# Optimization experiments

Hardware: AMD Instinct MI355X
Metric: run time of the kernel (lower is better)

The kernel has to match this reference:

```python
import jax, jax.numpy as jnp
import numpy as np


def setup_inputs() -> dict:
    key = jax.random.key(0)
    ks = jax.random.split(key, 4)
    C = 64
    return {
        "x": jax.random.normal(ks[0], (8, 64, 32, 32, 96), jnp.float32),
        "w_sr": jax.random.normal(ks[1], (64,), jnp.float32) * 0.1,
        "b_sr": jnp.zeros((64,), jnp.float32),
        "Wq": jax.random.normal(ks[2], (64, 64), jnp.float32) / np.sqrt(C),
        "bq": jnp.zeros((64,), jnp.float32),
        "Wkv": jax.random.normal(ks[3], (128, 64), jnp.float32) / np.sqrt(C),
        "bkv": jnp.zeros((128,), jnp.float32),
        "gamma": jnp.ones((4,), jnp.float32),
        "beta": jnp.zeros((4,), jnp.float32),
    }


def reference(x, w_sr, b_sr, Wq, bq, Wkv, bkv, gamma, beta):
    B, C, H, W, D = x.shape
    NH = gamma.shape[0]
    hd = C // NH
    scale = hd ** -0.5

    # 1x1x1 conv projections == channel matmuls
    q = jnp.einsum('oc,bchwd->bohwd', Wq, x) + bq[None, :, None, None, None]
    # sr_conv with sr_ratio=1 is a depthwise 1x1x1 conv: per-channel scale+shift
    kvin = x * w_sr[None, :, None, None, None] + b_sr[None, :, None, None, None]
    kv = jnp.einsum('oc,bchwd->bohwd', Wkv, kvin) + bkv[None, :, None, None, None]
    k, v = kv[:, :C], kv[:, C:]

    q = q.reshape(B, NH, hd, H, W, D)
    k = k.reshape(B, NH, hd, H, W, D)
    v = v.reshape(B, NH, hd, H, W, D)

    # Manhattan decay: spatial_dist[i,j] = |i-j| + |j-i| = 2|i-j| (H==W);
    # spectral_dist is identically zero in the original (d_idx.T is a no-op on 1D).
    idx = jnp.arange(H, dtype=x.dtype)
    dist = 2.0 * jnp.abs(idx[:, None] - idx[None, :])              # (H, H)
    dec = dist[None, :, :, None] * gamma[:, None, None, None] + beta[:, None, None, None]  # (NH,H,H,1)
    decay = jnp.exp(-jax.nn.softplus(dec))                          # broadcasts over D

    # matmul contracts over W; head_dim c is batch-like (faithful to original permutes)
    attn = jnp.einsum('bnchwd,bncgwd->bnchgd', q, k) * scale        # (B,NH,hd,H,H,D)
    attn = attn + decay[None, :, None]                               # (1,NH,1,H,H,1)
    attn = jax.nn.softmax(attn, axis=-1)                             # softmax over spectral D
    out = jnp.einsum('bnchgd,bncgjd->bnchjd', attn, v)               # (B,NH,hd,H,W,D)
    return out.reshape(B, C, H, W, D)
```

## Files before the change

kernel.cpp:

```cpp
#include <hip/hip_runtime.h>
#include <stdint.h>
#include <stddef.h>

typedef __attribute__((ext_vector_type(8))) short short8;
typedef __attribute__((ext_vector_type(4))) float f32x4;

#define PER_BO 98304

__device__ __forceinline__ unsigned int cvtpk(float lo, float hi) {
    unsigned int r;
    asm("v_cvt_pk_bf16_f32 %0, %1, %2" : "=v"(r) : "v"(lo), "v"(hi));
    return r;
}

__global__ __launch_bounds__(512, 2) void proj_mfma(
    const float* __restrict__ x, const float* __restrict__ w_sr, const float* __restrict__ b_sr,
    const float* __restrict__ Wq, const float* __restrict__ bq,
    const float* __restrict__ Wkv, const float* __restrict__ bkv,
    unsigned short* __restrict__ qb, unsigned short* __restrict__ kb, unsigned short* __restrict__ vb)
{
    __shared__ unsigned short Wh[12288];
    __shared__ float bl[192];
    __shared__ unsigned short Cb[2 * 6208];

    int t = threadIdx.x;
    int bidx = blockIdx.x;
    int b = bidx & 7;
    int dg = (bidx >> 3) & 7;
    int hrow = bidx >> 6;

    int lane = t & 63;
    int wvi = t >> 6;
    int lr = lane & 15, hk = lane >> 4;

    const float* xb = x + (size_t)b * 6291456 + hrow * 3072 + dg * 12;
    float af[3][16];
#pragma unroll
    for (int pi = 0; pi < 3; ++pi) {
        int m = (wvi * 3 + pi) * 16 + lr;
        int w = m / 12, dd = m - w * 12;
        const float* xp = xb + (size_t)(hk * 8) * 98304 + w * 96 + dd;
#pragma unroll
        for (int j = 0; j < 8; ++j) {
            af[pi][j]     = xp[(size_t)j * 98304];
            af[pi][8 + j] = xp[(size_t)(32 + j) * 98304];
        }
    }

#pragma unroll
    for (int i = 0; i < 6; ++i) {
        int qi = t + i * 512;
        int o = qi >> 4;
        int cq = qi & 15;
        int c = cq * 4;
        float4 wv4;
        if (o < 64) wv4 = *reinterpret_cast<const float4*>(Wq + o * 64 + c);
        else {
            wv4 = *reinterpret_cast<const float4*>(Wkv + (o - 64) * 64 + c);
            float4 sr = *reinterpret_cast<const float4*>(w_sr + c);
            wv4.x *= sr.x; wv4.y *= sr.y; wv4.z *= sr.z; wv4.w *= sr.w;
        }
        uint2 pk; pk.x = cvtpk(wv4.x, wv4.y); pk.y = cvtpk(wv4.z, wv4.w);
        int sw = (cq >> 1) ^ (o & 7);
        *reinterpret_cast<uint2*>(&Wh[o * 64 + sw * 8 + (cq & 1) * 4]) = pk;
    }
    if (t < 192) {
        float s;
        if (t < 64) s = bq[t];
        else {
            s = bkv[t - 64];
            for (int c = 0; c < 64; ++c) s += Wkv[(t - 64) * 64 + c] * b_sr[c];
        }
        bl[t] = s;
    }
    __syncthreads();

    short8 ahf[3][2], alf[3][2];
#pragma unroll
    for (int pi = 0; pi < 3; ++pi) {
#pragma unroll
        for (int half = 0; half < 2; ++half) {
            union { unsigned int u[4]; short8 v; } H, L;
#pragma unroll
            for (int q = 0; q < 4; ++q) {
                float f0 = af[pi][half * 8 + 2 * q];
                float f1 = af[pi][half * 8 + 2 * q + 1];
                unsigned int hp = cvtpk(f0, f1);
                float h0 = __uint_as_float(hp << 16);
                float h1 = __uint_as_float(hp & 0xffff0000u);
                H.u[q] = hp;
                L.u[q] = cvtpk(f0 - h0, f1 - h1);
            }
            ahf[pi][half] = H.v; alf[pi][half] = L.v;
        }
    }

    int wo[3];
#pragma unroll
    for (int pi = 0; pi < 3; ++pi)
        wo[pi] = lr * 388 + (wvi * 3 + pi) * 16 + hk * 4;

    int so_po[3], so_lo[3];
#pragma unroll
    for (int i = 0; i < 3; ++i) {
        int flat = i * 512 + t;
        int o_l = flat / 96;
        int rem = flat - o_l * 96;
        int dd = rem >> 3;
        int w4 = rem & 7;
        so_po[i] = o_l * PER_BO + dd * 1024 + w4 * 4;
        so_lo[i] = o_l * 388 + w4 * 48 + dd;
    }

    float biasv[12];
#pragma unroll
    for (int ot = 0; ot < 12; ++ot) biasv[ot] = bl[ot * 16 + lr];

    f32x4 zero4 = {0.f, 0.f, 0.f, 0.f};
    int s7 = lr & 7;

#pragma unroll
    for (int ot = 0; ot < 12; ++ot) {
        unsigned short* cb = Cb + (ot & 1) * 6208;
        {
            int o = ot * 16 + lr;
            const unsigned short* wr = &Wh[o * 64];
            short8 b0 = *reinterpret_cast<const short8*>(wr + ((hk ^ s7) * 8));
            short8 b1 = *reinterpret_cast<const short8*>(wr + (((hk + 4) ^ s7) * 8));
            float bo = biasv[ot];
#pragma unroll
            for (int pi = 0; pi < 3; ++pi) {
                f32x4 acc = __builtin_amdgcn_mfma_f32_16x16x32_bf16(ahf[pi][0], b0, zero4, 0, 0, 0);
                acc = __builtin_amdgcn_mfma_f32_16x16x32_bf16(ahf[pi][1], b1, acc, 0, 0, 0);
                acc = __builtin_amdgcn_mfma_f32_16x16x32_bf16(alf[pi][0], b0, acc, 0, 0, 0);
                acc = __builtin_amdgcn_mfma_f32_16x16x32_bf16(alf[pi][1], b1, acc, 0, 0, 0);
                uint2 st;
                st.x = cvtpk(acc[0] + bo, acc[1] + bo);
                st.y = cvtpk(acc[2] + bo, acc[3] + bo);
                *reinterpret_cast<uint2*>(&cb[wo[pi]]) = st;
            }
        }
        __syncthreads();
        {
            int sel = ot >> 2;
            unsigned short* base =
                (sel == 0 ? qb : (sel == 1 ? kb : vb))
                + (size_t)(b * 64 + (ot & 3) * 16) * PER_BO + dg * 12288 + hrow * 32;
#pragma unroll
            for (int i = 0; i < 3; ++i) {
                const unsigned short* c = &cb[so_lo[i]];
                uint2 v;
                v.x = (unsigned int)c[0]  | ((unsigned int)c[12] << 16);
                v.y = (unsigned int)c[24] | ((unsigned int)c[36] << 16);
                *reinterpret_cast<uint2*>(base + so_po[i]) = v;
            }
        }
    }
}

__global__ __launch_bounds__(512, 4) void attn_kernel(
    const unsigned short* __restrict__ qb, const unsigned short* __restrict__ kb,
    const unsigned short* __restrict__ vb,
    const float* __restrict__ gamma, const float* __restrict__ beta,
    float* __restrict__ out)
{
    __shared__ char smem[61440];
    unsigned short* Vw = (unsigned short*)smem;
    unsigned short* Pb = (unsigned short*)(smem + 18432);
    float* Osf  = (float*)(smem + 27648);
    float* lred = (float*)(smem + 27648);
    float* rlb  = (float*)(smem + 27648 + 16896);

    int t = threadIdx.x;
    int l = t & 63;
    int dsub = t >> 6;
    int lr = l & 15, hk = l >> 4;

    int id = blockIdx.x;
    int xcd = id & 7;
    int k7 = id >> 3;
    int p = xcd + 8 * (k7 >> 1);
    int half = k7 & 1;
    int oc = p & 63;
    int b = p >> 6;
    int n = oc >> 4;

    const unsigned short* qp = qb + (size_t)(b * 64 + oc) * PER_BO;
    const unsigned short* kp = kb + (size_t)(b * 64 + oc) * PER_BO;
    const unsigned short* vp = vb + (size_t)(b * 64 + oc) * PER_BO;

    float gm = gamma[n], bt = beta[n];
    float decv[8];
#pragma unroll
    for (int gb = 0; gb < 2; ++gb)
#pragma unroll
        for (int r = 0; r < 4; ++r) {
            int hh = half * 16 + hk * 4 + r;
            int gg = gb * 16 + lr;
            float dc = 2.0f * fabsf((float)(hh - gg)) * gm + bt;
            float sp = fmaxf(dc, 0.0f) + log1pf(__expf(-fabsf(dc)));
            decv[gb * 4 + r] = __expf(-sp);
        }

    const float scale = 0.25f;
    f32x4 zero4 = {0.f, 0.f, 0.f, 0.f};

    unsigned int ep[48];
    float lacc[8] = {0.f, 0.f, 0.f, 0.f, 0.f, 0.f, 0.f, 0.f};

    int qoff  = half * 512 + lr * 32 + hk * 8;
    int koff0 = lr * 32 + hk * 8;
    int koff1 = koff0 + 512;

    uint4 qv[2], k0v[2], k1v[2];
    {
        int b0p = dsub * 1024;
        qv[0]  = *reinterpret_cast<const uint4*>(qp + b0p + qoff);
        k0v[0] = *reinterpret_cast<const uint4*>(kp + b0p + koff0);
        k1v[0] = *reinterpret_cast<const uint4*>(kp + b0p + koff1);
        int b1p = (8 + dsub) * 1024;
        qv[1]  = *reinterpret_cast<const uint4*>(qp + b1p + qoff);
        k0v[1] = *reinterpret_cast<const uint4*>(kp + b1p + koff0);
        k1v[1] = *reinterpret_cast<const uint4*>(kp + b1p + koff1);
    }

#pragma unroll
    for (int ch = 0; ch < 12; ++ch) {
        int s = ch & 1;
        union { uint4 u; short8 v; } A, B0, B1;
        A.u = qv[s]; B0.u = k0v[s]; B1.u = k1v[s];
        f32x4 s0 = __builtin_amdgcn_mfma_f32_16x16x32_bf16(A.v, B0.v, zero4, 0, 0, 0);
        f32x4 s1 = __builtin_amdgcn_mfma_f32_16x16x32_bf16(A.v, B1.v, zero4, 0, 0, 0);
        if (ch < 10) {
            int bp = ((ch + 2) * 8 + dsub) * 1024;
            qv[s]  = *reinterpret_cast<const uint4*>(qp + bp + qoff);
            k0v[s] = *reinterpret_cast<const uint4*>(kp + bp + koff0);
            k1v[s] = *reinterpret_cast<const uint4*>(kp + bp + koff1);
        }
        float e[8];
#pragma unroll
        for (int r = 0; r < 4; ++r) {
            e[r]     = __expf(s0[r] * scale + decv[r]);
            e[4 + r] = __expf(s1[r] * scale + decv[4 + r]);
        }
#pragma unroll
        for (int i = 0; i < 8; ++i) lacc[i] += e[i];
        ep[ch * 4 + 0] = cvtpk(e[0], e[1]);
        ep[ch * 4 + 1] = cvtpk(e[2], e[3]);
        ep[ch * 4 + 2] = cvtpk(e[4], e[5]);
        ep[ch * 4 + 3] = cvtpk(e[6], e[7]);
    }

#pragma unroll
    for (int i = 0; i < 8; ++i)
        lred[dsub * 528 + (hk * 4 + (i & 3)) * 33 + (i >> 2) * 16 + lr] = lacc[i];
    __syncthreads();
    {
        float rsum = 0.f;
#pragma unroll
        for (int s = 0; s < 8; ++s) rsum += lred[s * 528 + (t >> 5) * 33 + (t & 31)];
        rlb[(t >> 5) * 33 + (t & 31)] = 1.0f / rsum;
    }
    __syncthreads();
    float rl8[8];
#pragma unroll
    for (int i = 0; i < 8; ++i)
        rl8[i] = rlb[(hk * 4 + (i & 3)) * 33 + (i >> 2) * 16 + lr];
    __syncthreads();

    int vgoff = l * 16;
    int vwbase = dsub * 1152 + ((l & 1) * 16) * 36 + (l >> 1);
    unsigned short* Pw = Pb + dsub * 576;

    uint4 vv0[2], vv1[2];
    {
        int b0p = dsub * 1024 + vgoff;
        vv0[0] = *reinterpret_cast<const uint4*>(vp + b0p);
        vv1[0] = *reinterpret_cast<const uint4*>(vp + b0p + 8);
        int b1p = (8 + dsub) * 1024 + vgoff;
        vv0[1] = *reinterpret_cast<const uint4*>(vp + b1p);
        vv1[1] = *reinterpret_cast<const uint4*>(vp + b1p + 8);
    }

    size_t obase0 = ((size_t)(b * 64 + oc) * 1024 + half * 512 + t) * 96;

#pragma unroll
    for (int ch = 0; ch < 12; ++ch) {
        int s = ch & 1;
        {
            union { uint4 u; unsigned short e[8]; } V0, V1;
            V0.u = vv0[s]; V1.u = vv1[s];
#pragma unroll
            for (int i = 0; i < 8; ++i) Vw[vwbase + i * 36] = V0.e[i];
#pragma unroll
            for (int i = 0; i < 8; ++i) Vw[vwbase + (i + 8) * 36] = V1.e[i];
        }
#pragma unroll
        for (int gb = 0; gb < 2; ++gb)
#pragma unroll
            for (int rp = 0; rp < 2; ++rp) {
                unsigned int u = ep[ch * 4 + gb * 2 + rp];
                float p0 = __uint_as_float(u << 16)         * rl8[gb * 4 + rp * 2];
                float p1 = __uint_as_float(u & 0xffff0000u) * rl8[gb * 4 + rp * 2 + 1];
                unsigned int pk = cvtpk(p0, p1);
                Pw[(hk * 4 + rp * 2) * 36 + gb * 16 + lr]     = (unsigned short)pk;
                Pw[(hk * 4 + rp * 2 + 1) * 36 + gb * 16 + lr] = (unsigned short)(pk >> 16);
            }
        if (ch < 10) {
            int bp = ((ch + 2) * 8 + dsub) * 1024 + vgoff;
            vv0[s] = *reinterpret_cast<const uint4*>(vp + bp);
            vv1[s] = *reinterpret_cast<const uint4*>(vp + bp + 8);
        }
        asm volatile("s_waitcnt lgkmcnt(0)" ::: "memory");
        __builtin_amdgcn_sched_barrier(0);
        short8 pa  = *reinterpret_cast<const short8*>(Pw + lr * 36 + hk * 8);
        short8 vb0 = *reinterpret_cast<const short8*>(Vw + dsub * 1152 + lr * 36 + hk * 8);
        short8 vb1 = *reinterpret_cast<const short8*>(Vw + dsub * 1152 + (16 + lr) * 36 + hk * 8);
        f32x4 o0 = __builtin_amdgcn_mfma_f32_16x16x32_bf16(pa, vb0, zero4, 0, 0, 0);
        f32x4 o1 = __builtin_amdgcn_mfma_f32_16x16x32_bf16(pa, vb1, zero4, 0, 0, 0);
        float* Od = Osf + s * 4224 + dsub * 528;
#pragma unroll
        for (int r = 0; r < 4; ++r) {
            Od[(hk * 4 + r) * 33 + lr]      = o0[r];
            Od[(hk * 4 + r) * 33 + 16 + lr] = o1[r];
        }
        if (ch & 1) {
            __syncthreads();
            int lidx = (t >> 5) * 33 + (t & 31);
            float4 q0, q1, q2, q3;
            q0.x = Osf[0 * 528 + lidx]; q0.y = Osf[1 * 528 + lidx];
            q0.z = Osf[2 * 528 + lidx]; q0.w = Osf[3 * 528 + lidx];
            q1.x = Osf[4 * 528 + lidx]; q1.y = Osf[5 * 528 + lidx];
            q1.z = Osf[6 * 528 + lidx]; q1.w = Osf[7 * 528 + lidx];
            q2.x = Osf[4224 + 0 * 528 + lidx]; q2.y = Osf[4224 + 1 * 528 + lidx];
            q2.z = Osf[4224 + 2 * 528 + lidx]; q2.w = Osf[4224 + 3 * 528 + lidx];
            q3.x = Osf[4224 + 4 * 528 + lidx]; q3.y = Osf[4224 + 5 * 528 + lidx];
            q3.z = Osf[4224 + 6 * 528 + lidx]; q3.w = Osf[4224 + 7 * 528 + lidx];
            float* po = out + obase0 + (ch >> 1) * 16;
            *reinterpret_cast<float4*>(po)      = q0;
            *reinterpret_cast<float4*>(po + 4)  = q1;
            *reinterpret_cast<float4*>(po + 8)  = q2;
            *reinterpret_cast<float4*>(po + 12) = q3;
            __syncthreads();
        }
    }
}

extern "C" void kernel_launch(void* const* d_in, const int* in_sizes, int n_in,
                              void* d_out, int out_size, void* d_ws, size_t ws_size,
                              hipStream_t stream) {
    const float* x     = (const float*)d_in[0];
    const float* w_sr  = (const float*)d_in[1];
    const float* b_sr  = (const float*)d_in[2];
    const float* Wq    = (const float*)d_in[3];
    const float* bq    = (const float*)d_in[4];
    const float* Wkv   = (const float*)d_in[5];
    const float* bkv   = (const float*)d_in[6];
    const float* gamma = (const float*)d_in[7];
    const float* beta  = (const float*)d_in[8];
    float* out = (float*)d_out;

    unsigned short* qb = (unsigned short*)d_ws;
    unsigned short* kb = qb + (size_t)50331648;
    unsigned short* vb = kb + (size_t)50331648;

    proj_mfma<<<2048, 512, 0, stream>>>(x, w_sr, b_sr, Wq, bq, Wkv, bkv, qb, kb, vb);

    attn_kernel<<<1024, 512, 0, stream>>>(qb, kb, vb, gamma, beta, out);
}
```

Baseline: 323.9 us.

## Retile projection kernel to 1024-thread blocks with 16-wide D tiles and 128-bit stores

The projection kernel now uses 1024-thread blocks, each covering 16 spectral positions by 32 W columns, instead of 512 threads covering 12 positions. With this tile shape each thread can gather 8 bf16 outputs from the LDS staging buffer and write them as a single 16-byte store, replacing the earlier 8-byte scattered stores. The goal is better coalescing of the bf16 Q/K/V writes and less index arithmetic. The LDS staging buffer grows. The aggressive launch bounds may push the compiler to limit registers, with a risk of spills.

```diff
diff --git a/kernel.cpp b/kernel.cpp
--- a/kernel.cpp
+++ b/kernel.cpp
@@ -13,7 +13,7 @@
     return r;
 }
 
-__global__ __launch_bounds__(512, 2) void proj_mfma(
+__global__ __launch_bounds__(1024, 8) void proj_mfma(
     const float* __restrict__ x, const float* __restrict__ w_sr, const float* __restrict__ b_sr,
     const float* __restrict__ Wq, const float* __restrict__ bq,
     const float* __restrict__ Wkv, const float* __restrict__ bkv,
@@ -21,25 +21,25 @@
 {
     __shared__ unsigned short Wh[12288];
     __shared__ float bl[192];
-    __shared__ unsigned short Cb[2 * 6208];
+    __shared__ unsigned short Cb[2 * 8256];
 
     int t = threadIdx.x;
     int bidx = blockIdx.x;
     int b = bidx & 7;
-    int dg = (bidx >> 3) & 7;
-    int hrow = bidx >> 6;
+    int r2 = bidx >> 3;
+    int hrow = r2 & 31;
+    int dg = r2 >> 5;
 
     int lane = t & 63;
     int wvi = t >> 6;
     int lr = lane & 15, hk = lane >> 4;
 
-    const float* xb = x + (size_t)b * 6291456 + hrow * 3072 + dg * 12;
-    float af[3][16];
-#pragma unroll
-    for (int pi = 0; pi < 3; ++pi) {
-        int m = (wvi * 3 + pi) * 16 + lr;
-        int w = m / 12, dd = m - w * 12;
-        const float* xp = xb + (size_t)(hk * 8) * 98304 + w * 96 + dd;
+    const float* xb = x + (size_t)b * 6291456 + hrow * 3072 + dg * 16;
+    float af[2][16];
+#pragma unroll
+    for (int pi = 0; pi < 2; ++pi) {
+        int w = wvi * 2 + pi;
+        const float* xp = xb + (size_t)(hk * 8) * 98304 + w * 96 + lr;
 #pragma unroll
         for (int j = 0; j < 8; ++j) {
             af[pi][j]     = xp[(size_t)j * 98304];
@@ -48,8 +48,8 @@
     }
 
 #pragma unroll
-    for (int i = 0; i < 6; ++i) {
-        int qi = t + i * 512;
+    for (int i = 0; i < 3; ++i) {
+        int qi = t + i * 1024;
         int o = qi >> 4;
         int cq = qi & 15;
         int c = cq * 4;
@@ -75,9 +75,9 @@
     }
     __syncthreads();
 
-    short8 ahf[3][2], alf[3][2];
-#pragma unroll
-    for (int pi = 0; pi < 3; ++pi) {
+    short8 ahf[2][2], alf[2][2];
+#pragma unroll
+    for (int pi = 0; pi < 2; ++pi) {
 #pragma unroll
         for (int half = 0; half < 2; ++half) {
             union { unsigned int u[4]; short8 v; } H, L;
@@ -95,22 +95,16 @@
         }
     }
 
-    int wo[3];
-#pragma unroll
-    for (int pi = 0; pi < 3; ++pi)
-        wo[pi] = lr * 388 + (wvi * 3 + pi) * 16 + hk * 4;
-
-    int so_po[3], so_lo[3];
-#pragma unroll
-    for (int i = 0; i < 3; ++i) {
-        int flat = i * 512 + t;
-        int o_l = flat / 96;
-        int rem = flat - o_l * 96;
-        int dd = rem >> 3;
-        int w4 = rem & 7;
-        so_po[i] = o_l * PER_BO + dd * 1024 + w4 * 4;
-        so_lo[i] = o_l * 388 + w4 * 48 + dd;
-    }
+    int wo[2];
+#pragma unroll
+    for (int pi = 0; pi < 2; ++pi)
+        wo[pi] = lr * 516 + (wvi * 2 + pi) * 16 + hk * 4;
+
+    int o_l = t >> 6;
+    int dd  = (t >> 2) & 15;
+    int w8  = t & 3;
+    size_t so_po = (size_t)o_l * PER_BO + (size_t)(dg * 16 + dd) * 1024 + hrow * 32 + w8 * 8;
+    int so_lo = o_l * 516 + w8 * 128 + dd;
 
     float biasv[12];
 #pragma unroll
@@ -121,7 +115,7 @@
 
 #pragma unroll
     for (int ot = 0; ot < 12; ++ot) {
-        unsigned short* cb = Cb + (ot & 1) * 6208;
+        unsigned short* cb = Cb + (ot & 1) * 8256;
         {
             int o = ot * 16 + lr;
             const unsigned short* wr = &Wh[o * 64];
@@ -129,7 +123,7 @@
             short8 b1 = *reinterpret_cast<const short8*>(wr + (((hk + 4) ^ s7) * 8));
             float bo = biasv[ot];
 #pragma unroll
-            for (int pi = 0; pi < 3; ++pi) {
+            for (int pi = 0; pi < 2; ++pi) {
                 f32x4 acc = __builtin_amdgcn_mfma_f32_16x16x32_bf16(ahf[pi][0], b0, zero4, 0, 0, 0);
                 acc = __builtin_amdgcn_mfma_f32_16x16x32_bf16(ahf[pi][1], b1, acc, 0, 0, 0);
                 acc = __builtin_amdgcn_mfma_f32_16x16x32_bf16(alf[pi][0], b0, acc, 0, 0, 0);
@@ -144,16 +138,11 @@
         {
             int sel = ot >> 2;
             unsigned short* base =
-                (sel == 0 ? qb : (sel == 1 ? kb : vb))
-                + (size_t)(b * 64 + (ot & 3) * 16) * PER_BO + dg * 12288 + hrow * 32;
-#pragma unroll
-            for (int i = 0; i < 3; ++i) {
-                const unsigned short* c = &cb[so_lo[i]];
-                uint2 v;
-                v.x = (unsigned int)c[0]  | ((unsigned int)c[12] << 16);
-                v.y = (unsigned int)c[24] | ((unsigned int)c[36] << 16);
-                *reinterpret_cast<uint2*>(base + so_po[i]) = v;
-            }
+                (sel == 0 ? qb : (sel == 1 ? kb : vb)) + (size_t)(b * 64 + (ot & 3) * 16) * PER_BO;
+            union { unsigned short e[8]; uint4 v; } pk;
+#pragma unroll
+            for (int k = 0; k < 8; ++k) pk.e[k] = cb[so_lo + k * 16];
+            *reinterpret_cast<uint4*>(base + so_po) = pk.v;
         }
     }
 }
@@ -364,7 +353,7 @@
     unsigned short* kb = qb + (size_t)50331648;
     unsigned short* vb = kb + (size_t)50331648;
 
-    proj_mfma<<<2048, 512, 0, stream>>>(x, w_sr, b_sr, Wq, bq, Wkv, bkv, qb, kb, vb);
+    proj_mfma<<<1536, 1024, 0, stream>>>(x, w_sr, b_sr, Wq, bq, Wkv, bkv, qb, kb, vb);
 
     attn_kernel<<<1024, 512, 0, stream>>>(qb, kb, vb, gamma, beta, out);
 }
```

New measurement: 385.3 us. 19.0% more time.
